# Performance work log

Hardware: AMD Instinct MI355X
Metric: run time of the kernel (lower is better)

Reference implementation:

```python
import jax, jax.numpy as jnp
import numpy as np
import math

B = 1024
G = 34  # grid_dim = 17*2
C = 4
SCENT = 19


def _scent_kernel_np():
    h = w = SCENT
    mx, my = 0.5 * h, 0.5 * w
    sx, sy = h / 4.0, w / 4.0
    x = np.linspace(0.0, h, h)
    y = np.linspace(0.0, w, w)
    X, Y = np.meshgrid(x, y, indexing='ij')
    z = (1.0 / (2.0 * math.pi * sx * sy)) * np.exp(-(((X - mx) ** 2) / (2 * sx ** 2) + ((Y - my) ** 2) / (2 * sy ** 2)))
    return (z * 80.0).astype(np.float32)


def setup_inputs() -> dict:
    key = jax.random.key(0)
    k1, k2, k3, k4 = jax.random.split(key, 4)
    cell = jax.random.uniform(k1, (B, C, G, G), dtype=jnp.float32)
    food = (jax.random.uniform(k2, (B, G, G), dtype=jnp.float32) > 0.97).astype(jnp.float32)
    fc1_w = jax.random.normal(k3, (64, 12), dtype=jnp.float32) * (1.0 / np.sqrt(12))
    fc1_b = jnp.zeros((64,), dtype=jnp.float32)
    fc2_w = jax.random.normal(k4, (4, 64), dtype=jnp.float32) * (1.0 / np.sqrt(64))
    fc2_b = jnp.zeros((4,), dtype=jnp.float32)
    scent_kernel = jnp.asarray(_scent_kernel_np())
    return {"cell": cell, "food": food, "fc1_w": fc1_w, "fc1_b": fc1_b,
            "fc2_w": fc2_w, "fc2_b": fc2_b, "scent_kernel": scent_kernel, "steps": 32}


def _conv(x, w, pad, groups):
    # x: [B, Cin, H, W], w: [Cout, Cin/groups, kh, kw]; cross-correlation like torch
    return jax.lax.conv_general_dilated(
        x, w, window_strides=(1, 1), padding=[(pad, pad), (pad, pad)],
        feature_group_count=groups, dimension_numbers=('NCHW', 'OIHW', 'NCHW'))


def _maxpool3(x):
    # 3x3 max pool, stride 1, pad 1 (pad value -inf, matching torch MaxPool2d semantics)
    return jax.lax.reduce_window(x, -jnp.inf, jax.lax.max, (1, 1, 3, 3), (1, 1, 1, 1),
                                 [(0, 0), (0, 0), (1, 1), (1, 1)])


def _forward(cell, food, fc1_w, fc1_b, fc2_w, fc2_b, scent_kernel, steps):
    dx = jnp.outer(jnp.array([1., 2., 1.], jnp.float32), jnp.array([-1., 0., 1.], jnp.float32)) / 8.0
    dy = dx.T
    kdx = jnp.tile(dx[None, None], (4, 1, 1, 1))  # depthwise, groups=4
    kdy = jnp.tile(dy[None, None], (4, 1, 1, 1))

    # perceive_scent: 19x19 gaussian conv, padding 9
    scent = _conv(food[:, None], scent_kernel[None, None], 9, 1)[:, 0]  # [B,G,G]

    def step(cell, _):
        cell = cell.at[:, 3].set(scent)
        # current living count per batch (cells in channel 0 above 0.8)
        cl = jnp.sum((cell[:, 0] > 0.8).astype(jnp.float32), axis=(1, 2))
        pre_mask = _maxpool3(cell[:, 0:1]) > 0.1  # [B,1,G,G]
        # perception: x, sobel-x, sobel-y -> 12 channels
        y1 = _conv(cell, kdx, 1, 4)
        y2 = _conv(cell, kdy, 1, 4)
        y = jnp.concatenate([cell, y1, y2], axis=1)  # [B,12,G,G]
        # tiny MLP per pixel (torch transposes dims 1<->3; linear over channels is equivalent)
        h = jax.nn.relu(jnp.einsum('bchw,oc->bohw', y, fc1_w) + fc1_b[None, :, None, None])
        upd = jnp.einsum('bchw,oc->bohw', h, fc2_w) + fc2_b[None, :, None, None]
        x = cell + upd
        post_mask = _maxpool3(x[:, 0:1]) > 0.1
        x = x * (pre_mask & post_mask).astype(x.dtype)
        x = jnp.clip(x, -10.0, 10.0)
        x = x.at[:, 0].set(jnp.clip(x[:, 0], 0.0, 1.0))
        # keep_k_largest: threshold = cl-th smallest (ascending sort index == cl); keep strictly greater
        flat = x[:, 0].reshape(B, -1)  # [B, G*G]
        srt = jnp.sort(flat, axis=1)
        kth = jnp.take_along_axis(srt, cl.astype(jnp.int32)[:, None], axis=1)  # [B,1] (gather clamps OOB)
        flat = jnp.where(flat > kth, flat, 0.0)
        x = x.at[:, 0].set(flat.reshape(B, G, G))
        return x, None

    cell, _ = jax.lax.scan(jax.checkpoint(step), cell, None, length=steps)
    total_pixel_val = cell[:, 0:1].sum(axis=(1, 2, 3))
    living_count = jnp.sum((cell[:, 0:1] > 0.1).astype(jnp.float32), axis=(1, 2, 3))
    return cell, food, total_pixel_val, living_count


def reference(cell, food, fc1_w, fc1_b, fc2_w, fc2_b, scent_kernel, steps):
    return _forward(cell, food, fc1_w, fc1_b, fc2_w, fc2_b, scent_kernel, steps)
```

## Files before the change

kernel.cpp:

```cpp
#include <hip/hip_runtime.h>
#include <stdint.h>

#define GD    34
#define RS    39
#define C0N   (38*RS)
#define CBN   (36*RS)
#define NPIX  1156
#define NT    256
#define NB    1024
#define TPR   7
#define TUSED 238
#define FS    57
#define SCRN  2960

#define SCAN_PASS(KK) do {                                                         \
    if (wid == 0) {                                                                \
      const int base2 = lane << 4;                                                 \
      int c16[16]; int csum = 0;                                                   \
      _Pragma("unroll")                                                            \
      for (int j = 0; j < 16; ++j) { c16[j] = hist[base2+j]; hist[base2+j] = 0; csum += c16[j]; } \
      int inc = csum;                                                              \
      _Pragma("unroll")                                                            \
      for (int off2 = 1; off2 < 64; off2 <<= 1) { int vv = __shfl_up(inc, off2); if (lane >= off2) inc += vv; } \
      const int excl = inc - csum;                                                 \
      if ((KK) >= excl && (KK) < inc) {                                            \
        int rem = (KK) - excl; int cum = 0;                                        \
        _Pragma("unroll")                                                          \
        for (int j = 0; j < 16; ++j) {                                             \
          if (rem >= cum && rem < cum + c16[j]) { sel_bin = base2 + j; sel_rem = rem - cum; } \
          cum += c16[j];                                                           \
        }                                                                          \
      }                                                                            \
    }                                                                              \
  } while (0)

__global__ __launch_bounds__(NT) __attribute__((amdgpu_waves_per_eu(4, 4)))
void ca_kernel(const float* __restrict__ cell_in,
               const float* __restrict__ food_in,
               const float* __restrict__ fc1_w,
               const float* __restrict__ fc1_b,
               const float* __restrict__ fc2_w,
               const float* __restrict__ fc2_b,
               const float* __restrict__ sk_g,
               const int*   __restrict__ steps_p,
               float* __restrict__ out)
{
  __shared__ float c0b[C0N];
  __shared__ float cbuf1[CBN];
  __shared__ float cbuf2[CBN];
  __shared__ float scratch[SCRN];
  __shared__ int   icl[2][4];
  __shared__ int   inzaz[4];
  __shared__ int   sel_bin, sel_rem;
  __shared__ float fsum[4];
  __shared__ int   lcnt[4];

  float* x0buf = scratch;
  int*   hist  = (int*)scratch;

  const int tid  = threadIdx.x;
  const int b    = blockIdx.x;
  const int lane = tid & 63;
  const int wid  = tid >> 6;
  const int nsteps = steps_p[0];

  const bool tval = (tid < TUSED);
  const int  trow = tval ? (tid / TPR) : 0;
  const int  c0   = tval ? ((tid % TPR) * 5) : 0;
  const int  nval = tval ? ((c0 <= 29) ? 5 : 4) : 0;
  const int  pb0c = (trow+2)*RS + c0 + 2;
  const int  pb1  = (trow+1)*RS + c0 + 1;
  const int  p0   = trow*GD + c0;
  const int  wb0  = trow*RS + c0;

  for (int idx = tid; idx < C0N;  idx += NT) c0b[idx]   = 0.f;
  for (int idx = tid; idx < CBN;  idx += NT) cbuf1[idx] = 0.f;
  for (int idx = tid; idx < CBN;  idx += NT) cbuf2[idx] = 0.f;
  for (int idx = tid; idx < SCRN; idx += NT) scratch[idx] = 0.f;
  __syncthreads();

  float v3k[5], v1k[5], v2k[5];
  int cnt0 = 0;
#pragma unroll
  for (int j = 0; j < 5; ++j) {
    v3k[j] = 0.f; v1k[j] = 0.f; v2k[j] = 0.f;
    if (j < nval) {
      int p = p0 + j;
      const float* gi = cell_in + (size_t)b*4*NPIX + p;
      float v0 = gi[0], v1 = gi[NPIX], v2 = gi[2*NPIX], v3 = gi[3*NPIX];
      c0b[pb0c+j] = v0; cbuf1[pb1+j] = v1; cbuf2[pb1+j] = v2;
      v3k[j] = v3;
      cnt0 += (v0 > 0.8f) ? 1 : 0;
      scratch[(trow+9)*FS + (c0+j+9)] = food_in[(size_t)b*NPIX + p];
    }
  }
#pragma unroll
  for (int off = 32; off; off >>= 1) cnt0 += __shfl_down(cnt0, off);
  if (lane == 0) icl[0][wid] = cnt0;
  __syncthreads();

  float scent[5] = {0.f, 0.f, 0.f, 0.f, 0.f};
  for (int dr = 0; dr < 19; ++dr) {
    const float* frow = scratch + (trow+dr)*FS + c0;
    float f[23];
#pragma unroll
    for (int q = 0; q < 23; ++q) f[q] = frow[q];
    const float* krow = sk_g + dr*19;
#pragma unroll
    for (int dc = 0; dc < 19; ++dc) {
      const float kv = krow[dc];
      scent[0] = fmaf(f[dc+0], kv, scent[0]);
      scent[1] = fmaf(f[dc+1], kv, scent[1]);
      scent[2] = fmaf(f[dc+2], kv, scent[2]);
      scent[3] = fmaf(f[dc+3], kv, scent[3]);
      scent[4] = fmaf(f[dc+4], kv, scent[4]);
    }
  }
  __syncthreads();
  for (int idx = tid; idx < SCRN; idx += NT) scratch[idx] = 0.f;
  __syncthreads();
#pragma unroll
  for (int j = 0; j < 5; ++j) if (j < nval) x0buf[pb1+j] = scent[j];
  __syncthreads();
  float sxs[5], sys[5];
#pragma unroll
  for (int j = 0; j < 5; ++j) {
    const int bb = (j < nval) ? (pb1 + j) : pb1;
    float t00=x0buf[bb-RS-1], t01=x0buf[bb-RS], t02=x0buf[bb-RS+1];
    float t10=x0buf[bb-1],                      t12=x0buf[bb+1];
    float t20=x0buf[bb+RS-1], t21=x0buf[bb+RS], t22=x0buf[bb+RS+1];
    sxs[j] = ((t02 - t00) + 2.f*(t12 - t10) + (t22 - t20)) * 0.125f;
    sys[j] = ((t20 - t00) + 2.f*(t21 - t01) + (t22 - t02)) * 0.125f;
  }

  const float b2r0 = fc2_b[0], b2r1 = fc2_b[1], b2r2 = fc2_b[2], b2r3 = fc2_b[3];

  for (int s = 0; s < nsteps; ++s) {
    __syncthreads();
    float r0[7], r1[7], r2[7], m3[9], m5[9];
    {
      m3[0] = c0b[wb0 + RS];
#pragma unroll
      for (int i = 0; i < 7; ++i) { r0[i] = c0b[wb0 + RS + 1 + i]; m3[i+1] = r0[i]; }
      m3[8] = c0b[wb0 + RS + 8];
      m3[0] = fmaxf(m3[0], c0b[wb0 + 2*RS]);
#pragma unroll
      for (int i = 0; i < 7; ++i) { r1[i] = c0b[wb0 + 2*RS + 1 + i]; m3[i+1] = fmaxf(m3[i+1], r1[i]); }
      m3[8] = fmaxf(m3[8], c0b[wb0 + 2*RS + 8]);
      m3[0] = fmaxf(m3[0], c0b[wb0 + 3*RS]);
#pragma unroll
      for (int i = 0; i < 7; ++i) { r2[i] = c0b[wb0 + 3*RS + 1 + i]; m3[i+1] = fmaxf(m3[i+1], r2[i]); }
      m3[8] = fmaxf(m3[8], c0b[wb0 + 3*RS + 8]);
#pragma unroll
      for (int q = 0; q < 9; ++q) m5[q] = fmaxf(fmaxf(c0b[wb0 + q], m3[q]), c0b[wb0 + 4*RS + q]);
    }
    unsigned pm = 0, am = 0;
#pragma unroll
    for (int j = 0; j < 5; ++j) {
      if (j < nval) {
        if (fmaxf(fmaxf(m3[j+1], m3[j+2]), m3[j+3]) > 0.1f) pm |= (1u << j);
        float mm5 = fmaxf(fmaxf(fmaxf(fmaxf(m5[j], m5[j+1]), m5[j+2]), m5[j+3]), m5[j+4]);
        if (mm5 > 0.1f) am |= (1u << j);
      }
    }
#pragma unroll
    for (int j = 0; j < 5; ++j) {
      int acti = (j < nval) ? (int)((am >> j) & 1u) : 0;
      if (__any(acti)) {
        const int bb = pb1 + j;
        const float y0 = r1[j+1];
        const float y4 = ((r0[j+2] - r0[j]) + 2.f*(r1[j+2] - r1[j]) + (r2[j+2] - r2[j])) * 0.125f;
        const float y8 = ((r2[j] - r0[j]) + 2.f*(r2[j+1] - r0[j+1]) + (r2[j+2] - r0[j+2])) * 0.125f;
        float y1, y5, y9, y2, y6, y10;
        {
          const float* cb = cbuf1;
          float t00=cb[bb-RS-1], t01=cb[bb-RS], t02=cb[bb-RS+1];
          float t10=cb[bb-1],    t11=cb[bb],    t12=cb[bb+1];
          float t20=cb[bb+RS-1], t21=cb[bb+RS], t22=cb[bb+RS+1];
          y1 = t11;
          y5 = ((t02 - t00) + 2.f*(t12 - t10) + (t22 - t20)) * 0.125f;
          y9 = ((t20 - t00) + 2.f*(t21 - t01) + (t22 - t02)) * 0.125f;
        }
        {
          const float* cb = cbuf2;
          float t00=cb[bb-RS-1], t01=cb[bb-RS], t02=cb[bb-RS+1];
          float t10=cb[bb-1],    t11=cb[bb],    t12=cb[bb+1];
          float t20=cb[bb+RS-1], t21=cb[bb+RS], t22=cb[bb+RS+1];
          y2 = t11;
          y6 = ((t02 - t00) + 2.f*(t12 - t10) + (t22 - t20)) * 0.125f;
          y10= ((t20 - t00) + 2.f*(t21 - t01) + (t22 - t02)) * 0.125f;
        }
        const float y3 = scent[j], y7 = sxs[j], y11 = sys[j];
        float u0 = b2r0, u1 = b2r1, u2 = b2r2, u3 = b2r3;
        for (int o = 0; o < 64; ++o) {
          const float* wr = fc1_w + o*12;
          float t = fc1_b[o];
          t = fmaf(y0, wr[0], t);  t = fmaf(y1, wr[1], t);
          t = fmaf(y2, wr[2], t);  t = fmaf(y3, wr[3], t);
          t = fmaf(y4, wr[4], t);  t = fmaf(y5, wr[5], t);
          t = fmaf(y6, wr[6], t);  t = fmaf(y7, wr[7], t);
          t = fmaf(y8, wr[8], t);  t = fmaf(y9, wr[9], t);
          t = fmaf(y10, wr[10], t); t = fmaf(y11, wr[11], t);
          t = fmaxf(t, 0.f);
          u0 = fmaf(t, fc2_w[o],     u0);
          u1 = fmaf(t, fc2_w[64+o],  u1);
          u2 = fmaf(t, fc2_w[128+o], u2);
          u3 = fmaf(t, fc2_w[192+o], u3);
        }
        v3k[j] = y3 + u3;
        if (j < nval) {
          x0buf[bb]  = y0 + u0;
          v1k[j]     = y1 + u1;
          v2k[j]     = y2 + u2;
        }
      }
    }
    __syncthreads();
    unsigned pq = 0;
    float midv[5];
#pragma unroll
    for (int j = 0; j < 5; ++j) midv[j] = 0.f;
    if (pm) {
      float dm[7];
#pragma unroll
      for (int jc = 0; jc < 7; ++jc) {
        dm[jc] = 0.f;
        if (jc < nval + 2) {
          const int a = pb1 - 1 + jc;
          float u = x0buf[a-RS], m = x0buf[a], d = x0buf[a+RS];
          dm[jc] = fmaxf(fmaxf(u, m), d);
          if (jc >= 1 && jc <= 5) midv[jc-1] = m;
        }
      }
#pragma unroll
      for (int j = 0; j < 5; ++j)
        if (fmaxf(fmaxf(dm[j], dm[j+1]), dm[j+2]) > 0.1f) pq |= (1u << j);
    }
    int packed = 0;
    float v0s[5];
#pragma unroll
    for (int j = 0; j < 5; ++j) {
      v0s[j] = 0.f;
      if (j < nval) {
        bool alive = ((pm >> j) & 1u) && ((pq >> j) & 1u);
        float v0 = 0.f, v1 = 0.f, v2 = 0.f, v3 = 0.f;
        if (alive) {
          v0 = fminf(fmaxf(midv[j],   0.f),  1.f);
          v1 = fminf(fmaxf(v1k[j],  -10.f), 10.f);
          v2 = fminf(fmaxf(v2k[j],  -10.f), 10.f);
          v3 = fminf(fmaxf(v3k[j],  -10.f), 10.f);
        }
        cbuf1[pb1+j] = v1; cbuf2[pb1+j] = v2; v3k[j] = v3;
        v0s[j] = v0;
        int zer = (v0 == 0.f) ? 1 : 0;
        int azf = (zer && v1 == 0.f && v2 == 0.f && v3 == 0.f) ? 1 : 0;
        packed += zer + (azf << 16);
      }
    }
#pragma unroll
    for (int off = 32; off; off >>= 1) packed += __shfl_down(packed, off);
    if (lane == 0) inzaz[wid] = packed;
    __syncthreads();
    const int t01 = inzaz[0]+inzaz[1]+inzaz[2]+inzaz[3];
    const int nz = t01 & 0xffff, az = t01 >> 16;
    const int cl = icl[s&1][0]+icl[s&1][1]+icl[s&1][2]+icl[s&1][3];
    const int k  = (cl < NPIX) ? cl : (NPIX-1);
    float kth = 0.f;
    if (k >= nz) {
      hist[tid] = 0; hist[tid+256] = 0; hist[tid+512] = 0; hist[tid+768] = 0;
      __syncthreads();
      const int k2 = k - nz;
#pragma unroll
      for (int j = 0; j < 5; ++j) {
        unsigned u = __float_as_uint(v0s[j]);
        if (j < nval && u != 0u) atomicAdd(&hist[u >> 20], 1);
      }
      __syncthreads();
      SCAN_PASS(k2);
      __syncthreads();
      const int bin1 = sel_bin; const int kr2 = sel_rem;
#pragma unroll
      for (int j = 0; j < 5; ++j) {
        unsigned u = __float_as_uint(v0s[j]);
        if (j < nval && u != 0u && (u >> 20) == (unsigned)bin1)
          atomicAdd(&hist[(u >> 10) & 1023u], 1);
      }
      __syncthreads();
      SCAN_PASS(kr2);
      __syncthreads();
      const int bin2 = sel_bin; const int kr3 = sel_rem;
      const unsigned pref2 = (((unsigned)bin1) << 10) | (unsigned)bin2;
#pragma unroll
      for (int j = 0; j < 5; ++j) {
        unsigned u = __float_as_uint(v0s[j]);
        if (j < nval && u != 0u && (u >> 10) == pref2)
          atomicAdd(&hist[u & 1023u], 1);
      }
      __syncthreads();
      SCAN_PASS(kr3);
      __syncthreads();
      kth = __uint_as_float((((unsigned)bin1) << 20) | (((unsigned)bin2) << 10) | (unsigned)sel_bin);
    }
    int cnt = 0;
#pragma unroll
    for (int j = 0; j < 5; ++j) {
      if (j < nval) {
        float w0 = (v0s[j] > kth) ? v0s[j] : 0.f;
        c0b[pb0c+j] = w0;
        cnt += (w0 > 0.8f) ? 1 : 0;
      }
    }
#pragma unroll
    for (int off = 32; off; off >>= 1) cnt += __shfl_down(cnt, off);
    if (lane == 0) icl[(s+1)&1][wid] = cnt;
    if (az == NPIX) break;
  }

  const size_t CELL_N = (size_t)4*NPIX*NB;
  const size_t FOOD_N = (size_t)NPIX*NB;
  float tp = 0.f; int lcv = 0;
#pragma unroll
  for (int j = 0; j < 5; ++j) {
    if (j < nval) {
      const int p = p0 + j;
      float c0v = c0b[pb0c+j], c1 = cbuf1[pb1+j], c2 = cbuf2[pb1+j];
      size_t go = (size_t)b*4*NPIX + p;
      out[go]          = c0v;
      out[go +   NPIX] = c1;
      out[go + 2*NPIX] = c2;
      out[go + 3*NPIX] = v3k[j];
      out[CELL_N + (size_t)b*NPIX + p] = food_in[(size_t)b*NPIX + p];
      tp += c0v;
      lcv += (c0v > 0.1f) ? 1 : 0;
    }
  }
#pragma unroll
  for (int off = 32; off; off >>= 1) { tp += __shfl_down(tp, off); lcv += __shfl_down(lcv, off); }
  if (lane == 0) { fsum[wid] = tp; lcnt[wid] = lcv; }
  __syncthreads();
  if (tid == 0) {
    out[CELL_N + FOOD_N + b]      = fsum[0]+fsum[1]+fsum[2]+fsum[3];
    out[CELL_N + FOOD_N + NB + b] = (float)(lcnt[0]+lcnt[1]+lcnt[2]+lcnt[3]);
  }
}

extern "C" void kernel_launch(void* const* d_in, const int* in_sizes, int n_in,
                              void* d_out, int out_size, void* d_ws, size_t ws_size,
                              hipStream_t stream) {
  const float* cell  = (const float*)d_in[0];
  const float* food  = (const float*)d_in[1];
  const float* fc1w  = (const float*)d_in[2];
  const float* fc1b  = (const float*)d_in[3];
  const float* fc2w  = (const float*)d_in[4];
  const float* fc2b  = (const float*)d_in[5];
  const float* sk    = (const float*)d_in[6];
  const int*   steps = (const int*)d_in[7];
  float* out = (float*)d_out;
  ca_kernel<<<NB, NT, 0, stream>>>(cell, food, fc1w, fc1b, fc2w, fc2b, sk, steps, out);
}
```

Baseline: 236.7 us.

## Compact active pixels into a shared list and run MLP over compacted work

Replaces the per-thread, wave-uniform __any loop over five owned pixels with stream compaction. Active pixels are written to a shared list through a wave prefix sum and an atomic counter, then threads take list entries strided by thread ID and run the perception stencil and MLP. This removes the divergence waste from waves where only a few lanes have active pixels. In exchange it adds shared buffers for the per-step outputs, recomputes the scent gradient inside each step, uses more LDS, and drops the waves_per_eu attribute.

```diff
diff --git a/kernel.cpp b/kernel.cpp
--- a/kernel.cpp
+++ b/kernel.cpp
@@ -3,15 +3,23 @@
 
 #define GD    34
 #define RS    39
-#define C0N   (38*RS)
-#define CBN   (36*RS)
 #define NPIX  1156
 #define NT    256
 #define NB    1024
 #define TPR   7
 #define TUSED 238
 #define FS    57
-#define SCRN  2960
+
+#define O_C0B 0
+#define O_CB1 1482
+#define O_CB2 2886
+#define O_SCH 4290
+#define O_X0  5694
+#define O_X1  7098
+#define O_X2  8254
+#define O_X3  9410
+#define O_AL  10566
+#define POOLN 11726
 
 #define SCAN_PASS(KK) do {                                                         \
     if (wid == 0) {                                                                \
@@ -19,11 +27,11 @@
       int c16[16]; int csum = 0;                                                   \
       _Pragma("unroll")                                                            \
       for (int j = 0; j < 16; ++j) { c16[j] = hist[base2+j]; hist[base2+j] = 0; csum += c16[j]; } \
-      int inc = csum;                                                              \
+      int inc2 = csum;                                                             \
       _Pragma("unroll")                                                            \
-      for (int off2 = 1; off2 < 64; off2 <<= 1) { int vv = __shfl_up(inc, off2); if (lane >= off2) inc += vv; } \
-      const int excl = inc - csum;                                                 \
-      if ((KK) >= excl && (KK) < inc) {                                            \
+      for (int off2 = 1; off2 < 64; off2 <<= 1) { int vv = __shfl_up(inc2, off2); if (lane >= off2) inc2 += vv; } \
+      const int excl = inc2 - csum;                                                \
+      if ((KK) >= excl && (KK) < inc2) {                                           \
         int rem = (KK) - excl; int cum = 0;                                        \
         _Pragma("unroll")                                                          \
         for (int j = 0; j < 16; ++j) {                                             \
@@ -34,7 +42,7 @@
     }                                                                              \
   } while (0)
 
-__global__ __launch_bounds__(NT) __attribute__((amdgpu_waves_per_eu(4, 4)))
+__global__ __launch_bounds__(NT)
 void ca_kernel(const float* __restrict__ cell_in,
                const float* __restrict__ food_in,
                const float* __restrict__ fc1_w,
@@ -45,18 +53,25 @@
                const int*   __restrict__ steps_p,
                float* __restrict__ out)
 {
-  __shared__ float c0b[C0N];
-  __shared__ float cbuf1[CBN];
-  __shared__ float cbuf2[CBN];
-  __shared__ float scratch[SCRN];
+  __shared__ float pool[POOLN];
   __shared__ int   icl[2][4];
   __shared__ int   inzaz[4];
   __shared__ int   sel_bin, sel_rem;
+  __shared__ int   ctr;
   __shared__ float fsum[4];
   __shared__ int   lcnt[4];
 
-  float* x0buf = scratch;
-  int*   hist  = (int*)scratch;
+  float* c0b   = pool + O_C0B;
+  float* cb1   = pool + O_CB1;
+  float* cb2   = pool + O_CB2;
+  float* sch   = pool + O_SCH;
+  float* x0p   = pool + O_X0;
+  float* x1p   = pool + O_X1;
+  float* x2p   = pool + O_X2;
+  float* x3p   = pool + O_X3;
+  int*   alist = (int*)(pool + O_AL);
+  int*   hist  = (int*)(pool + O_AL);
+  float* foodc = pool + O_X0;
 
   const int tid  = threadIdx.x;
   const int b    = blockIdx.x;
@@ -73,25 +88,22 @@
   const int  p0   = trow*GD + c0;
   const int  wb0  = trow*RS + c0;
 
-  for (int idx = tid; idx < C0N;  idx += NT) c0b[idx]   = 0.f;
-  for (int idx = tid; idx < CBN;  idx += NT) cbuf1[idx] = 0.f;
-  for (int idx = tid; idx < CBN;  idx += NT) cbuf2[idx] = 0.f;
-  for (int idx = tid; idx < SCRN; idx += NT) scratch[idx] = 0.f;
+  for (int idx = tid; idx < POOLN; idx += NT) pool[idx] = 0.f;
   __syncthreads();
 
-  float v3k[5], v1k[5], v2k[5];
+  float v3k[5];
   int cnt0 = 0;
 #pragma unroll
   for (int j = 0; j < 5; ++j) {
-    v3k[j] = 0.f; v1k[j] = 0.f; v2k[j] = 0.f;
+    v3k[j] = 0.f;
     if (j < nval) {
       int p = p0 + j;
       const float* gi = cell_in + (size_t)b*4*NPIX + p;
       float v0 = gi[0], v1 = gi[NPIX], v2 = gi[2*NPIX], v3 = gi[3*NPIX];
-      c0b[pb0c+j] = v0; cbuf1[pb1+j] = v1; cbuf2[pb1+j] = v2;
+      c0b[pb0c+j] = v0; cb1[pb1+j] = v1; cb2[pb1+j] = v2;
       v3k[j] = v3;
       cnt0 += (v0 > 0.8f) ? 1 : 0;
-      scratch[(trow+9)*FS + (c0+j+9)] = food_in[(size_t)b*NPIX + p];
+      foodc[(trow+9)*FS + (c0+j+9)] = food_in[(size_t)b*NPIX + p];
     }
   }
 #pragma unroll
@@ -101,7 +113,7 @@
 
   float scent[5] = {0.f, 0.f, 0.f, 0.f, 0.f};
   for (int dr = 0; dr < 19; ++dr) {
-    const float* frow = scratch + (trow+dr)*FS + c0;
+    const float* frow = foodc + (trow+dr)*FS + c0;
     float f[23];
 #pragma unroll
     for (int q = 0; q < 23; ++q) f[q] = frow[q];
@@ -117,43 +129,26 @@
     }
   }
   __syncthreads();
-  for (int idx = tid; idx < SCRN; idx += NT) scratch[idx] = 0.f;
-  __syncthreads();
-#pragma unroll
-  for (int j = 0; j < 5; ++j) if (j < nval) x0buf[pb1+j] = scent[j];
-  __syncthreads();
-  float sxs[5], sys[5];
-#pragma unroll
-  for (int j = 0; j < 5; ++j) {
-    const int bb = (j < nval) ? (pb1 + j) : pb1;
-    float t00=x0buf[bb-RS-1], t01=x0buf[bb-RS], t02=x0buf[bb-RS+1];
-    float t10=x0buf[bb-1],                      t12=x0buf[bb+1];
-    float t20=x0buf[bb+RS-1], t21=x0buf[bb+RS], t22=x0buf[bb+RS+1];
-    sxs[j] = ((t02 - t00) + 2.f*(t12 - t10) + (t22 - t20)) * 0.125f;
-    sys[j] = ((t20 - t00) + 2.f*(t21 - t01) + (t22 - t02)) * 0.125f;
-  }
+  for (int idx = tid; idx < 1404; idx += NT) x0p[idx] = 0.f;
+#pragma unroll
+  for (int j = 0; j < 5; ++j) if (j < nval) sch[pb1+j] = scent[j];
 
   const float b2r0 = fc2_b[0], b2r1 = fc2_b[1], b2r2 = fc2_b[2], b2r3 = fc2_b[3];
 
   for (int s = 0; s < nsteps; ++s) {
+    if (tid == 0) ctr = 0;
     __syncthreads();
-    float r0[7], r1[7], r2[7], m3[9], m5[9];
-    {
-      m3[0] = c0b[wb0 + RS];
-#pragma unroll
-      for (int i = 0; i < 7; ++i) { r0[i] = c0b[wb0 + RS + 1 + i]; m3[i+1] = r0[i]; }
-      m3[8] = c0b[wb0 + RS + 8];
-      m3[0] = fmaxf(m3[0], c0b[wb0 + 2*RS]);
-#pragma unroll
-      for (int i = 0; i < 7; ++i) { r1[i] = c0b[wb0 + 2*RS + 1 + i]; m3[i+1] = fmaxf(m3[i+1], r1[i]); }
-      m3[8] = fmaxf(m3[8], c0b[wb0 + 2*RS + 8]);
-      m3[0] = fmaxf(m3[0], c0b[wb0 + 3*RS]);
-#pragma unroll
-      for (int i = 0; i < 7; ++i) { r2[i] = c0b[wb0 + 3*RS + 1 + i]; m3[i+1] = fmaxf(m3[i+1], r2[i]); }
-      m3[8] = fmaxf(m3[8], c0b[wb0 + 3*RS + 8]);
-#pragma unroll
-      for (int q = 0; q < 9; ++q) m5[q] = fmaxf(fmaxf(c0b[wb0 + q], m3[q]), c0b[wb0 + 4*RS + q]);
-    }
+    float m3[9], m5[9];
+#pragma unroll
+    for (int q = 0; q < 9; ++q) m5[q] = c0b[wb0 + q];
+#pragma unroll
+    for (int q = 0; q < 9; ++q) m3[q] = c0b[wb0 + RS + q];
+#pragma unroll
+    for (int q = 0; q < 9; ++q) m3[q] = fmaxf(m3[q], c0b[wb0 + 2*RS + q]);
+#pragma unroll
+    for (int q = 0; q < 9; ++q) m3[q] = fmaxf(m3[q], c0b[wb0 + 3*RS + q]);
+#pragma unroll
+    for (int q = 0; q < 9; ++q) m5[q] = fmaxf(fmaxf(m5[q], m3[q]), c0b[wb0 + 4*RS + q]);
     unsigned pm = 0, am = 0;
 #pragma unroll
     for (int j = 0; j < 5; ++j) {
@@ -163,57 +158,84 @@
         if (mm5 > 0.1f) am |= (1u << j);
       }
     }
-#pragma unroll
-    for (int j = 0; j < 5; ++j) {
-      int acti = (j < nval) ? (int)((am >> j) & 1u) : 0;
-      if (__any(acti)) {
-        const int bb = pb1 + j;
-        const float y0 = r1[j+1];
-        const float y4 = ((r0[j+2] - r0[j]) + 2.f*(r1[j+2] - r1[j]) + (r2[j+2] - r2[j])) * 0.125f;
-        const float y8 = ((r2[j] - r0[j]) + 2.f*(r2[j+1] - r0[j+1]) + (r2[j+2] - r0[j+2])) * 0.125f;
-        float y1, y5, y9, y2, y6, y10;
-        {
-          const float* cb = cbuf1;
-          float t00=cb[bb-RS-1], t01=cb[bb-RS], t02=cb[bb-RS+1];
-          float t10=cb[bb-1],    t11=cb[bb],    t12=cb[bb+1];
-          float t20=cb[bb+RS-1], t21=cb[bb+RS], t22=cb[bb+RS+1];
-          y1 = t11;
-          y5 = ((t02 - t00) + 2.f*(t12 - t10) + (t22 - t20)) * 0.125f;
-          y9 = ((t20 - t00) + 2.f*(t21 - t01) + (t22 - t02)) * 0.125f;
-        }
-        {
-          const float* cb = cbuf2;
-          float t00=cb[bb-RS-1], t01=cb[bb-RS], t02=cb[bb-RS+1];
-          float t10=cb[bb-1],    t11=cb[bb],    t12=cb[bb+1];
-          float t20=cb[bb+RS-1], t21=cb[bb+RS], t22=cb[bb+RS+1];
-          y2 = t11;
-          y6 = ((t02 - t00) + 2.f*(t12 - t10) + (t22 - t20)) * 0.125f;
-          y10= ((t20 - t00) + 2.f*(t21 - t01) + (t22 - t02)) * 0.125f;
-        }
-        const float y3 = scent[j], y7 = sxs[j], y11 = sys[j];
-        float u0 = b2r0, u1 = b2r1, u2 = b2r2, u3 = b2r3;
-        for (int o = 0; o < 64; ++o) {
-          const float* wr = fc1_w + o*12;
-          float t = fc1_b[o];
-          t = fmaf(y0, wr[0], t);  t = fmaf(y1, wr[1], t);
-          t = fmaf(y2, wr[2], t);  t = fmaf(y3, wr[3], t);
-          t = fmaf(y4, wr[4], t);  t = fmaf(y5, wr[5], t);
-          t = fmaf(y6, wr[6], t);  t = fmaf(y7, wr[7], t);
-          t = fmaf(y8, wr[8], t);  t = fmaf(y9, wr[9], t);
-          t = fmaf(y10, wr[10], t); t = fmaf(y11, wr[11], t);
-          t = fmaxf(t, 0.f);
-          u0 = fmaf(t, fc2_w[o],     u0);
-          u1 = fmaf(t, fc2_w[64+o],  u1);
-          u2 = fmaf(t, fc2_w[128+o], u2);
-          u3 = fmaf(t, fc2_w[192+o], u3);
-        }
-        v3k[j] = y3 + u3;
-        if (j < nval) {
-          x0buf[bb]  = y0 + u0;
-          v1k[j]     = y1 + u1;
-          v2k[j]     = y2 + u2;
-        }
-      }
+    {
+      int k = __popc(am);
+      int inc = k;
+#pragma unroll
+      for (int off = 1; off < 64; off <<= 1) { int v = __shfl_up(inc, off); if (lane >= off) inc += v; }
+      int wtot = __shfl(inc, 63);
+      int basew = 0;
+      if (lane == 0 && wtot) basew = atomicAdd(&ctr, wtot);
+      basew = __shfl(basew, 0);
+      int woff = basew + inc - k;
+      unsigned bb = am;
+      while (bb) { int j = __ffs(bb) - 1; bb &= bb - 1; alist[woff++] = p0 + j; }
+    }
+    __syncthreads();
+    const int nact = ctr;
+    for (int it = tid; it < nact; it += NT) {
+      const int p  = alist[it];
+      const int r  = p / GD;
+      const int cc = p - r*GD;
+      const int g0 = (r+2)*RS + cc + 2;
+      const int h0 = (r+1)*RS + cc + 1;
+      float y0, y1, y2, y3, y4, y5, y6, y7, y8, y9, y10, y11;
+      {
+        const float* cb = c0b;
+        float t00=cb[g0-RS-1], t01=cb[g0-RS], t02=cb[g0-RS+1];
+        float t10=cb[g0-1],    t11=cb[g0],    t12=cb[g0+1];
+        float t20=cb[g0+RS-1], t21=cb[g0+RS], t22=cb[g0+RS+1];
+        y0 = t11;
+        y4 = ((t02 - t00) + 2.f*(t12 - t10) + (t22 - t20)) * 0.125f;
+        y8 = ((t20 - t00) + 2.f*(t21 - t01) + (t22 - t02)) * 0.125f;
+      }
+      {
+        const float* cb = cb1;
+        float t00=cb[h0-RS-1], t01=cb[h0-RS], t02=cb[h0-RS+1];
+        float t10=cb[h0-1],    t11=cb[h0],    t12=cb[h0+1];
+        float t20=cb[h0+RS-1], t21=cb[h0+RS], t22=cb[h0+RS+1];
+        y1 = t11;
+        y5 = ((t02 - t00) + 2.f*(t12 - t10) + (t22 - t20)) * 0.125f;
+        y9 = ((t20 - t00) + 2.f*(t21 - t01) + (t22 - t02)) * 0.125f;
+      }
+      {
+        const float* cb = cb2;
+        float t00=cb[h0-RS-1], t01=cb[h0-RS], t02=cb[h0-RS+1];
+        float t10=cb[h0-1],    t11=cb[h0],    t12=cb[h0+1];
+        float t20=cb[h0+RS-1], t21=cb[h0+RS], t22=cb[h0+RS+1];
+        y2 = t11;
+        y6 = ((t02 - t00) + 2.f*(t12 - t10) + (t22 - t20)) * 0.125f;
+        y10= ((t20 - t00) + 2.f*(t21 - t01) + (t22 - t02)) * 0.125f;
+      }
+      {
+        const float* cb = sch;
+        float t00=cb[h0-RS-1], t01=cb[h0-RS], t02=cb[h0-RS+1];
+        float t10=cb[h0-1],    t11=cb[h0],    t12=cb[h0+1];
+        float t20=cb[h0+RS-1], t21=cb[h0+RS], t22=cb[h0+RS+1];
+        y3 = t11;
+        y7 = ((t02 - t00) + 2.f*(t12 - t10) + (t22 - t20)) * 0.125f;
+        y11= ((t20 - t00) + 2.f*(t21 - t01) + (t22 - t02)) * 0.125f;
+      }
+      float u0 = b2r0, u1 = b2r1, u2 = b2r2, u3 = b2r3;
+      for (int o = 0; o < 64; ++o) {
+        const float* wr = fc1_w + o*12;
+        float t = fc1_b[o];
+        t = fmaf(y0, wr[0], t);  t = fmaf(y1, wr[1], t);
+        t = fmaf(y2, wr[2], t);  t = fmaf(y3, wr[3], t);
+        t = fmaf(y4, wr[4], t);  t = fmaf(y5, wr[5], t);
+        t = fmaf(y6, wr[6], t);  t = fmaf(y7, wr[7], t);
+        t = fmaf(y8, wr[8], t);  t = fmaf(y9, wr[9], t);
+        t = fmaf(y10, wr[10], t); t = fmaf(y11, wr[11], t);
+        t = fmaxf(t, 0.f);
+        u0 = fmaf(t, fc2_w[o],     u0);
+        u1 = fmaf(t, fc2_w[64+o],  u1);
+        u2 = fmaf(t, fc2_w[128+o], u2);
+        u3 = fmaf(t, fc2_w[192+o], u3);
+      }
+      x0p[h0] = y0 + u0;
+      x1p[p]  = y1 + u1;
+      x2p[p]  = y2 + u2;
+      x3p[p]  = y3 + u3;
     }
     __syncthreads();
     unsigned pq = 0;
@@ -227,7 +249,7 @@
         dm[jc] = 0.f;
         if (jc < nval + 2) {
           const int a = pb1 - 1 + jc;
-          float u = x0buf[a-RS], m = x0buf[a], d = x0buf[a+RS];
+          float u = x0p[a-RS], m = x0p[a], d = x0p[a+RS];
           dm[jc] = fmaxf(fmaxf(u, m), d);
           if (jc >= 1 && jc <= 5) midv[jc-1] = m;
         }
@@ -245,12 +267,12 @@
         bool alive = ((pm >> j) & 1u) && ((pq >> j) & 1u);
         float v0 = 0.f, v1 = 0.f, v2 = 0.f, v3 = 0.f;
         if (alive) {
-          v0 = fminf(fmaxf(midv[j],   0.f),  1.f);
-          v1 = fminf(fmaxf(v1k[j],  -10.f), 10.f);
-          v2 = fminf(fmaxf(v2k[j],  -10.f), 10.f);
-          v3 = fminf(fmaxf(v3k[j],  -10.f), 10.f);
+          v0 = fminf(fmaxf(midv[j],      0.f),  1.f);
+          v1 = fminf(fmaxf(x1p[p0+j], -10.f), 10.f);
+          v2 = fminf(fmaxf(x2p[p0+j], -10.f), 10.f);
+          v3 = fminf(fmaxf(x3p[p0+j], -10.f), 10.f);
         }
-        cbuf1[pb1+j] = v1; cbuf2[pb1+j] = v2; v3k[j] = v3;
+        cb1[pb1+j] = v1; cb2[pb1+j] = v2; v3k[j] = v3;
         v0s[j] = v0;
         int zer = (v0 == 0.f) ? 1 : 0;
         int azf = (zer && v1 == 0.f && v2 == 0.f && v3 == 0.f) ? 1 : 0;
@@ -323,7 +345,7 @@
   for (int j = 0; j < 5; ++j) {
     if (j < nval) {
       const int p = p0 + j;
-      float c0v = c0b[pb0c+j], c1 = cbuf1[pb1+j], c2 = cbuf2[pb1+j];
+      float c0v = c0b[pb0c+j], c1 = cb1[pb1+j], c2 = cb2[pb1+j];
       size_t go = (size_t)b*4*NPIX + p;
       out[go]          = c0v;
       out[go +   NPIX] = c1;
```

New measurement: 284.4 us. +20.1%, slower.

## Track alive cells with per-row 64-bit bitmasks instead of shared-memory max-pool reads

Applied to the files above, without the earlier changes.

Replaces the 3x3 and 5x5 max-pool liveness tests, which read a padded channel-0 buffer from shared memory, with per-row 64-bit alive bitmasks. Threads build the masks with atomicOr at each step and test neighbourhoods with bitwise ORs and shifts. Channel-0 neighbour rows are loaded only when some lane in the wave is active. The shared buffers are also merged into one pool with a shallower padding, which cuts LDS usage and may raise occupancy. The cost is extra atomics, a double-buffered mask array that must be cleared each step, and some added complexity.

```diff
diff --git a/kernel.cpp b/kernel.cpp
--- a/kernel.cpp
+++ b/kernel.cpp
@@ -3,7 +3,6 @@
 
 #define GD    34
 #define RS    39
-#define C0N   (38*RS)
 #define CBN   (36*RS)
 #define NPIX  1156
 #define NT    256
@@ -11,7 +10,12 @@
 #define TPR   7
 #define TUSED 238
 #define FS    57
-#define SCRN  2960
+
+#define O_C0B 0
+#define O_CB1 1404
+#define O_CB2 2808
+#define O_X0  4212
+#define POOLN 5616
 
 #define SCAN_PASS(KK) do {                                                         \
     if (wid == 0) {                                                                \
@@ -19,11 +23,11 @@
       int c16[16]; int csum = 0;                                                   \
       _Pragma("unroll")                                                            \
       for (int j = 0; j < 16; ++j) { c16[j] = hist[base2+j]; hist[base2+j] = 0; csum += c16[j]; } \
-      int inc = csum;                                                              \
+      int inc2 = csum;                                                             \
       _Pragma("unroll")                                                            \
-      for (int off2 = 1; off2 < 64; off2 <<= 1) { int vv = __shfl_up(inc, off2); if (lane >= off2) inc += vv; } \
-      const int excl = inc - csum;                                                 \
-      if ((KK) >= excl && (KK) < inc) {                                            \
+      for (int off2 = 1; off2 < 64; off2 <<= 1) { int vv = __shfl_up(inc2, off2); if (lane >= off2) inc2 += vv; } \
+      const int excl = inc2 - csum;                                                \
+      if ((KK) >= excl && (KK) < inc2) {                                           \
         int rem = (KK) - excl; int cum = 0;                                        \
         _Pragma("unroll")                                                          \
         for (int j = 0; j < 16; ++j) {                                             \
@@ -45,18 +49,20 @@
                const int*   __restrict__ steps_p,
                float* __restrict__ out)
 {
-  __shared__ float c0b[C0N];
-  __shared__ float cbuf1[CBN];
-  __shared__ float cbuf2[CBN];
-  __shared__ float scratch[SCRN];
+  __shared__ float pool[POOLN];
+  __shared__ unsigned long long avb[2][38];
   __shared__ int   icl[2][4];
   __shared__ int   inzaz[4];
   __shared__ int   sel_bin, sel_rem;
   __shared__ float fsum[4];
   __shared__ int   lcnt[4];
 
-  float* x0buf = scratch;
-  int*   hist  = (int*)scratch;
+  float* c0b  = pool + O_C0B;
+  float* cb1  = pool + O_CB1;
+  float* cb2  = pool + O_CB2;
+  float* x0p  = pool + O_X0;
+  int*   hist = (int*)(pool + O_X0);
+  float* foodc = pool;
 
   const int tid  = threadIdx.x;
   const int b    = blockIdx.x;
@@ -68,40 +74,22 @@
   const int  trow = tval ? (tid / TPR) : 0;
   const int  c0   = tval ? ((tid % TPR) * 5) : 0;
   const int  nval = tval ? ((c0 <= 29) ? 5 : 4) : 0;
-  const int  pb0c = (trow+2)*RS + c0 + 2;
   const int  pb1  = (trow+1)*RS + c0 + 1;
   const int  p0   = trow*GD + c0;
-  const int  wb0  = trow*RS + c0;
-
-  for (int idx = tid; idx < C0N;  idx += NT) c0b[idx]   = 0.f;
-  for (int idx = tid; idx < CBN;  idx += NT) cbuf1[idx] = 0.f;
-  for (int idx = tid; idx < CBN;  idx += NT) cbuf2[idx] = 0.f;
-  for (int idx = tid; idx < SCRN; idx += NT) scratch[idx] = 0.f;
-  __syncthreads();
-
-  float v3k[5], v1k[5], v2k[5];
-  int cnt0 = 0;
-#pragma unroll
-  for (int j = 0; j < 5; ++j) {
-    v3k[j] = 0.f; v1k[j] = 0.f; v2k[j] = 0.f;
-    if (j < nval) {
-      int p = p0 + j;
-      const float* gi = cell_in + (size_t)b*4*NPIX + p;
-      float v0 = gi[0], v1 = gi[NPIX], v2 = gi[2*NPIX], v3 = gi[3*NPIX];
-      c0b[pb0c+j] = v0; cbuf1[pb1+j] = v1; cbuf2[pb1+j] = v2;
-      v3k[j] = v3;
-      cnt0 += (v0 > 0.8f) ? 1 : 0;
-      scratch[(trow+9)*FS + (c0+j+9)] = food_in[(size_t)b*NPIX + p];
-    }
-  }
-#pragma unroll
-  for (int off = 32; off; off >>= 1) cnt0 += __shfl_down(cnt0, off);
-  if (lane == 0) icl[0][wid] = cnt0;
+  const int  wb   = trow*RS + c0;
+
+  for (int idx = tid; idx < POOLN; idx += NT) pool[idx] = 0.f;
+  for (int idx = tid; idx < 76;    idx += NT) ((unsigned long long*)avb)[idx] = 0ull;
+  __syncthreads();
+
+#pragma unroll
+  for (int j = 0; j < 5; ++j)
+    if (j < nval) foodc[(trow+9)*FS + (c0+j+9)] = food_in[(size_t)b*NPIX + p0 + j];
   __syncthreads();
 
   float scent[5] = {0.f, 0.f, 0.f, 0.f, 0.f};
   for (int dr = 0; dr < 19; ++dr) {
-    const float* frow = scratch + (trow+dr)*FS + c0;
+    const float* frow = foodc + (trow+dr)*FS + c0;
     float f[23];
 #pragma unroll
     for (int q = 0; q < 23; ++q) f[q] = frow[q];
@@ -117,18 +105,37 @@
     }
   }
   __syncthreads();
-  for (int idx = tid; idx < SCRN; idx += NT) scratch[idx] = 0.f;
-  __syncthreads();
-#pragma unroll
-  for (int j = 0; j < 5; ++j) if (j < nval) x0buf[pb1+j] = scent[j];
+  for (int idx = tid; idx < O_X0; idx += NT) pool[idx] = 0.f;
+  __syncthreads();
+
+  float v3k[5], v1k[5], v2k[5];
+  unsigned long long avm0 = 0ull;
+  int cnt0 = 0;
+#pragma unroll
+  for (int j = 0; j < 5; ++j) {
+    v3k[j] = 0.f; v1k[j] = 0.f; v2k[j] = 0.f;
+    if (j < nval) {
+      const float* gi = cell_in + (size_t)b*4*NPIX + p0 + j;
+      float v0 = gi[0], v1 = gi[NPIX], v2 = gi[2*NPIX], v3 = gi[3*NPIX];
+      c0b[pb1+j] = v0; cb1[pb1+j] = v1; cb2[pb1+j] = v2;
+      v3k[j] = v3;
+      cnt0 += (v0 > 0.8f) ? 1 : 0;
+      if (v0 > 0.1f) avm0 |= (1ull << j);
+      x0p[pb1+j] = scent[j];
+    }
+  }
+  if (avm0) atomicOr(&avb[0][trow+2], avm0 << (c0+2));
+#pragma unroll
+  for (int off = 32; off; off >>= 1) cnt0 += __shfl_down(cnt0, off);
+  if (lane == 0) icl[0][wid] = cnt0;
   __syncthreads();
   float sxs[5], sys[5];
 #pragma unroll
   for (int j = 0; j < 5; ++j) {
     const int bb = (j < nval) ? (pb1 + j) : pb1;
-    float t00=x0buf[bb-RS-1], t01=x0buf[bb-RS], t02=x0buf[bb-RS+1];
-    float t10=x0buf[bb-1],                      t12=x0buf[bb+1];
-    float t20=x0buf[bb+RS-1], t21=x0buf[bb+RS], t22=x0buf[bb+RS+1];
+    float t00=x0p[bb-RS-1], t01=x0p[bb-RS], t02=x0p[bb-RS+1];
+    float t10=x0p[bb-1],                    t12=x0p[bb+1];
+    float t20=x0p[bb+RS-1], t21=x0p[bb+RS], t22=x0p[bb+RS+1];
     sxs[j] = ((t02 - t00) + 2.f*(t12 - t10) + (t22 - t20)) * 0.125f;
     sys[j] = ((t20 - t00) + 2.f*(t21 - t01) + (t22 - t02)) * 0.125f;
   }
@@ -137,85 +144,82 @@
 
   for (int s = 0; s < nsteps; ++s) {
     __syncthreads();
-    float r0[7], r1[7], r2[7], m3[9], m5[9];
-    {
-      m3[0] = c0b[wb0 + RS];
-#pragma unroll
-      for (int i = 0; i < 7; ++i) { r0[i] = c0b[wb0 + RS + 1 + i]; m3[i+1] = r0[i]; }
-      m3[8] = c0b[wb0 + RS + 8];
-      m3[0] = fmaxf(m3[0], c0b[wb0 + 2*RS]);
-#pragma unroll
-      for (int i = 0; i < 7; ++i) { r1[i] = c0b[wb0 + 2*RS + 1 + i]; m3[i+1] = fmaxf(m3[i+1], r1[i]); }
-      m3[8] = fmaxf(m3[8], c0b[wb0 + 2*RS + 8]);
-      m3[0] = fmaxf(m3[0], c0b[wb0 + 3*RS]);
-#pragma unroll
-      for (int i = 0; i < 7; ++i) { r2[i] = c0b[wb0 + 3*RS + 1 + i]; m3[i+1] = fmaxf(m3[i+1], r2[i]); }
-      m3[8] = fmaxf(m3[8], c0b[wb0 + 3*RS + 8]);
-#pragma unroll
-      for (int q = 0; q < 9; ++q) m5[q] = fmaxf(fmaxf(c0b[wb0 + q], m3[q]), c0b[wb0 + 4*RS + q]);
-    }
+    const unsigned long long* av = avb[s&1];
+    const unsigned long long q0 = av[trow],   q1 = av[trow+1], q2 = av[trow+2],
+                             q3 = av[trow+3], q4 = av[trow+4];
+    const unsigned long long or3 = q1 | q2 | q3;
+    const unsigned long long or5 = or3 | q0 | q4;
     unsigned pm = 0, am = 0;
 #pragma unroll
     for (int j = 0; j < 5; ++j) {
       if (j < nval) {
-        if (fmaxf(fmaxf(m3[j+1], m3[j+2]), m3[j+3]) > 0.1f) pm |= (1u << j);
-        float mm5 = fmaxf(fmaxf(fmaxf(fmaxf(m5[j], m5[j+1]), m5[j+2]), m5[j+3]), m5[j+4]);
-        if (mm5 > 0.1f) am |= (1u << j);
-      }
-    }
-#pragma unroll
-    for (int j = 0; j < 5; ++j) {
-      int acti = (j < nval) ? (int)((am >> j) & 1u) : 0;
-      if (__any(acti)) {
-        const int bb = pb1 + j;
-        const float y0 = r1[j+1];
-        const float y4 = ((r0[j+2] - r0[j]) + 2.f*(r1[j+2] - r1[j]) + (r2[j+2] - r2[j])) * 0.125f;
-        const float y8 = ((r2[j] - r0[j]) + 2.f*(r2[j+1] - r0[j+1]) + (r2[j+2] - r0[j+2])) * 0.125f;
-        float y1, y5, y9, y2, y6, y10;
-        {
-          const float* cb = cbuf1;
-          float t00=cb[bb-RS-1], t01=cb[bb-RS], t02=cb[bb-RS+1];
-          float t10=cb[bb-1],    t11=cb[bb],    t12=cb[bb+1];
-          float t20=cb[bb+RS-1], t21=cb[bb+RS], t22=cb[bb+RS+1];
-          y1 = t11;
-          y5 = ((t02 - t00) + 2.f*(t12 - t10) + (t22 - t20)) * 0.125f;
-          y9 = ((t20 - t00) + 2.f*(t21 - t01) + (t22 - t02)) * 0.125f;
+        if ((or3 >> (c0+j+1)) & 7ull)  pm |= (1u << j);
+        if ((or5 >> (c0+j))   & 31ull) am |= (1u << j);
+      }
+    }
+    if (__any(am != 0u)) {
+      float r0[7], r1[7], r2[7];
+#pragma unroll
+      for (int q = 0; q < 7; ++q) r0[q] = c0b[wb + q];
+#pragma unroll
+      for (int q = 0; q < 7; ++q) r1[q] = c0b[wb + RS + q];
+#pragma unroll
+      for (int q = 0; q < 7; ++q) r2[q] = c0b[wb + 2*RS + q];
+#pragma unroll
+      for (int j = 0; j < 5; ++j) {
+        int acti = (j < nval) ? (int)((am >> j) & 1u) : 0;
+        if (__any(acti)) {
+          const int bb = pb1 + j;
+          const float y0 = r1[j+1];
+          const float y4 = ((r0[j+2] - r0[j]) + 2.f*(r1[j+2] - r1[j]) + (r2[j+2] - r2[j])) * 0.125f;
+          const float y8 = ((r2[j] - r0[j]) + 2.f*(r2[j+1] - r0[j+1]) + (r2[j+2] - r0[j+2])) * 0.125f;
+          float y1, y5, y9, y2, y6, y10;
+          {
+            const float* cb = cb1;
+            float t00=cb[bb-RS-1], t01=cb[bb-RS], t02=cb[bb-RS+1];
+            float t10=cb[bb-1],    t11=cb[bb],    t12=cb[bb+1];
+            float t20=cb[bb+RS-1], t21=cb[bb+RS], t22=cb[bb+RS+1];
+            y1 = t11;
+            y5 = ((t02 - t00) + 2.f*(t12 - t10) + (t22 - t20)) * 0.125f;
+            y9 = ((t20 - t00) + 2.f*(t21 - t01) + (t22 - t02)) * 0.125f;
+          }
+          {
+            const float* cb = cb2;
+            float t00=cb[bb-RS-1], t01=cb[bb-RS], t02=cb[bb-RS+1];
+            float t10=cb[bb-1],    t11=cb[bb],    t12=cb[bb+1];
+            float t20=cb[bb+RS-1], t21=cb[bb+RS], t22=cb[bb+RS+1];
+            y2 = t11;
+            y6 = ((t02 - t00) + 2.f*(t12 - t10) + (t22 - t20)) * 0.125f;
+            y10= ((t20 - t00) + 2.f*(t21 - t01) + (t22 - t02)) * 0.125f;
+          }
+          const float y3 = scent[j], y7 = sxs[j], y11 = sys[j];
+          float u0 = b2r0, u1 = b2r1, u2 = b2r2, u3 = b2r3;
+          for (int o = 0; o < 64; ++o) {
+            const float* wr = fc1_w + o*12;
+            float t = fc1_b[o];
+            t = fmaf(y0, wr[0], t);  t = fmaf(y1, wr[1], t);
+            t = fmaf(y2, wr[2], t);  t = fmaf(y3, wr[3], t);
+            t = fmaf(y4, wr[4], t);  t = fmaf(y5, wr[5], t);
+            t = fmaf(y6, wr[6], t);  t = fmaf(y7, wr[7], t);
+            t = fmaf(y8, wr[8], t);  t = fmaf(y9, wr[9], t);
+            t = fmaf(y10, wr[10], t); t = fmaf(y11, wr[11], t);
+            t = fmaxf(t, 0.f);
+            u0 = fmaf(t, fc2_w[o],     u0);
+            u1 = fmaf(t, fc2_w[64+o],  u1);
+            u2 = fmaf(t, fc2_w[128+o], u2);
+            u3 = fmaf(t, fc2_w[192+o], u3);
+          }
+          v3k[j] = y3 + u3;
+          if (j < nval) {
+            x0p[bb]  = y0 + u0;
+            v1k[j]   = y1 + u1;
+            v2k[j]   = y2 + u2;
+          }
         }
-        {
-          const float* cb = cbuf2;
-          float t00=cb[bb-RS-1], t01=cb[bb-RS], t02=cb[bb-RS+1];
-          float t10=cb[bb-1],    t11=cb[bb],    t12=cb[bb+1];
-          float t20=cb[bb+RS-1], t21=cb[bb+RS], t22=cb[bb+RS+1];
-          y2 = t11;
-          y6 = ((t02 - t00) + 2.f*(t12 - t10) + (t22 - t20)) * 0.125f;
-          y10= ((t20 - t00) + 2.f*(t21 - t01) + (t22 - t02)) * 0.125f;
-        }
-        const float y3 = scent[j], y7 = sxs[j], y11 = sys[j];
-        float u0 = b2r0, u1 = b2r1, u2 = b2r2, u3 = b2r3;
-        for (int o = 0; o < 64; ++o) {
-          const float* wr = fc1_w + o*12;
-          float t = fc1_b[o];
-          t = fmaf(y0, wr[0], t);  t = fmaf(y1, wr[1], t);
-          t = fmaf(y2, wr[2], t);  t = fmaf(y3, wr[3], t);
-          t = fmaf(y4, wr[4], t);  t = fmaf(y5, wr[5], t);
-          t = fmaf(y6, wr[6], t);  t = fmaf(y7, wr[7], t);
-          t = fmaf(y8, wr[8], t);  t = fmaf(y9, wr[9], t);
-          t = fmaf(y10, wr[10], t); t = fmaf(y11, wr[11], t);
-          t = fmaxf(t, 0.f);
-          u0 = fmaf(t, fc2_w[o],     u0);
-          u1 = fmaf(t, fc2_w[64+o],  u1);
-          u2 = fmaf(t, fc2_w[128+o], u2);
-          u3 = fmaf(t, fc2_w[192+o], u3);
-        }
-        v3k[j] = y3 + u3;
-        if (j < nval) {
-          x0buf[bb]  = y0 + u0;
-          v1k[j]     = y1 + u1;
-          v2k[j]     = y2 + u2;
-        }
       }
     }
     __syncthreads();
+    if (tid < 38) avb[s&1][tid] = 0ull;
     unsigned pq = 0;
     float midv[5];
 #pragma unroll
@@ -227,7 +231,7 @@
         dm[jc] = 0.f;
         if (jc < nval + 2) {
           const int a = pb1 - 1 + jc;
-          float u = x0buf[a-RS], m = x0buf[a], d = x0buf[a+RS];
+          float u = x0p[a-RS], m = x0p[a], d = x0p[a+RS];
           dm[jc] = fmaxf(fmaxf(u, m), d);
           if (jc >= 1 && jc <= 5) midv[jc-1] = m;
         }
@@ -250,7 +254,7 @@
           v2 = fminf(fmaxf(v2k[j],  -10.f), 10.f);
           v3 = fminf(fmaxf(v3k[j],  -10.f), 10.f);
         }
-        cbuf1[pb1+j] = v1; cbuf2[pb1+j] = v2; v3k[j] = v3;
+        cb1[pb1+j] = v1; cb2[pb1+j] = v2; v3k[j] = v3;
         v0s[j] = v0;
         int zer = (v0 == 0.f) ? 1 : 0;
         int azf = (zer && v1 == 0.f && v2 == 0.f && v3 == 0.f) ? 1 : 0;
@@ -301,15 +305,18 @@
       __syncthreads();
       kth = __uint_as_float((((unsigned)bin1) << 20) | (((unsigned)bin2) << 10) | (unsigned)sel_bin);
     }
+    unsigned long long avm = 0ull;
     int cnt = 0;
 #pragma unroll
     for (int j = 0; j < 5; ++j) {
       if (j < nval) {
         float w0 = (v0s[j] > kth) ? v0s[j] : 0.f;
-        c0b[pb0c+j] = w0;
+        c0b[pb1+j] = w0;
         cnt += (w0 > 0.8f) ? 1 : 0;
-      }
-    }
+        if (w0 > 0.1f) avm |= (1ull << j);
+      }
+    }
+    if (avm) atomicOr(&avb[(s+1)&1][trow+2], avm << (c0+2));
 #pragma unroll
     for (int off = 32; off; off >>= 1) cnt += __shfl_down(cnt, off);
     if (lane == 0) icl[(s+1)&1][wid] = cnt;
@@ -323,7 +330,7 @@
   for (int j = 0; j < 5; ++j) {
     if (j < nval) {
       const int p = p0 + j;
-      float c0v = c0b[pb0c+j], c1 = cbuf1[pb1+j], c2 = cbuf2[pb1+j];
+      float c0v = c0b[pb1+j], c1 = cb1[pb1+j], c2 = cb2[pb1+j];
       size_t go = (size_t)b*4*NPIX + p;
       out[go]          = c0v;
       out[go +   NPIX] = c1;
```

Result: faster. 231.1 us (-2.4%).
